# Kernel tuning notes

Measured on AMD Instinct MI355X. Metric: run time of the kernel, lower is better.

The kernel has to match this reference:

```python
import jax, jax.numpy as jnp
import numpy as np

BS, T, D, R = 8, 256, 2048, 4
N, K, G, GS, H = 8192, 64, 512, 16, 64
MOD_IN, MOD_OUT = K + 5, K + 2


def setup_inputs() -> dict:
    key = jax.random.key(0)
    ks = jax.random.split(key, 8)
    cc_signals = jax.random.normal(ks[0], (BS, T, D), dtype=jnp.float32)
    mod_w1 = jax.random.normal(ks[1], (G, MOD_IN, H), dtype=jnp.float32) * (2.0 / (MOD_IN + H)) ** 0.5
    mod_b1 = jnp.zeros((G, H), dtype=jnp.float32)
    mod_w2 = jax.random.normal(ks[2], (G, H, MOD_OUT), dtype=jnp.float32) * 0.01
    mod_b2 = jax.random.normal(ks[3], (G, MOD_OUT), dtype=jnp.float32) * 0.01
    conn_indices = jax.random.randint(ks[4], (N, K), 0, N, dtype=jnp.int32)
    conn_indices = jnp.sort(conn_indices, axis=-1)
    pos = jnp.arange(N, dtype=jnp.float32)
    neuron_id = jnp.stack([jnp.sin(pos * (2 * np.pi / N)), jnp.cos(pos * (2 * np.pi / N))], axis=-1)
    V0 = jax.random.normal(ks[5], (BS, N), dtype=jnp.float32) * 0.1
    activation0 = jax.nn.sigmoid(V0)
    hebbian0 = jnp.zeros((BS, N, K), dtype=jnp.float32)
    decay0 = jnp.full((BS, N), 0.9, dtype=jnp.float32)
    threshold0 = jnp.zeros((BS, N), dtype=jnp.float32)
    return {"cc_signals": cc_signals, "mod_w1": mod_w1, "mod_b1": mod_b1,
            "mod_w2": mod_w2, "mod_b2": mod_b2, "conn_indices": conn_indices,
            "neuron_id": neuron_id, "V0": V0, "activation0": activation0,
            "hebbian0": hebbian0, "decay0": decay0, "threshold0": threshold0}


def _modulator(activation, hebbian, decay, threshold, neuron_id, w1, b1, w2, b2):
    # [BS, N, K+5]
    nid = jnp.broadcast_to(neuron_id[None], (BS, N, 2))
    mod_in = jnp.concatenate([activation[..., None], hebbian, decay[..., None],
                              threshold[..., None], nid], axis=-1)
    x = mod_in.reshape(BS, G, GS, MOD_IN)
    hdn = jnp.tanh(jnp.einsum('bgsi,gih->bgsh', x, w1) + b1[None, :, None, :])
    out = jnp.einsum('bgsh,gho->bgso', hdn, w2) + b2[None, :, None, :]
    out = out.reshape(BS, N, MOD_OUT)
    return out[..., :K], jax.nn.sigmoid(out[..., K]), out[..., K + 1]


def reference(cc_signals, mod_w1, mod_b1, mod_w2, mod_b2, conn_indices, neuron_id,
              V0, activation0, hebbian0, decay0, threshold0):
    w_conn, decay, threshold = _modulator(activation0, hebbian0, decay0, threshold0,
                                          neuron_id, mod_w1, mod_b1, mod_w2, mod_b2)
    inject_all = jnp.repeat(cc_signals, R, axis=-1)  # [BS, T, N]

    def step(carry, inj_t):
        V, act, heb = carry
        nbr = act[:, conn_indices]                       # [BS, N, K] gather
        recv = jnp.sum(nbr * w_conn, axis=-1) + inj_t    # [BS, N]
        V = decay * V + (1.0 - decay) * recv
        act = jax.nn.sigmoid(V - threshold)
        heb = heb + act[..., None] * nbr
        return (V, act, heb), act

    heb_init = jnp.zeros((BS, N, K), dtype=V0.dtype)
    (_, _, _), acts = jax.lax.scan(step, (V0, activation0, heb_init),
                                   jnp.swapaxes(inject_all, 0, 1))
    act_all = jnp.swapaxes(acts, 0, 1)                   # [BS, T, N]
    mem_out = act_all.reshape(BS, T, D, R).mean(axis=-1)  # readout
    return mem_out
```

## Files before the change

### kernel.cpp

```cpp
#include <hip/hip_runtime.h>
#include <cstdint>
#include <cstddef>

#define BS 8
#define TT 256
#define DD 2048
#define NN 8192
#define KK 64
#define GG 512
#define GSZ 16
#define HH 64
#define MIN_ 69
#define MOUT_ 66
#define NSL 32
#define SLN 256
#define NW (NN/2)

typedef float    f32x4 __attribute__((ext_vector_type(4)));
typedef uint32_t u32x4 __attribute__((ext_vector_type(4)));

__global__ __launch_bounds__(256) void prep_kernel(
    const int* __restrict__ conn, int* __restrict__ ad_stored,
    unsigned char* __restrict__ inv2)
{
  const int gtid = blockIdx.x * 256 + threadIdx.x;
  const int n    = gtid >> 6;
  const int lane = gtid & 63;
  int idx  = conn[(size_t)n * KK + lane];
  int bank = (idx >> 1) & 31;
  unsigned key = ((unsigned)bank << 6) | (unsigned)lane;
  int rank = 0;
  #pragma unroll
  for (int i = 0; i < 64; ++i) {
    unsigned ki = (unsigned)__shfl((int)key, i);
    rank += (ki < key) ? 1 : 0;
  }
  const int ln = n & 63;
  const int r  = ((ln & 31) * 2 + (ln >> 5)) & 63;
  int j = (rank - r) & 63;
  ad_stored[(size_t)n * KK + j] = ((idx >> 1) << 2) | (idx & 1);
  inv2[(size_t)n * KK + lane]   = (unsigned char)j;
}

__global__ __launch_bounds__(256) void modulator_kernel(
    const float* __restrict__ w1, const float* __restrict__ b1,
    const float* __restrict__ w2, const float* __restrict__ b2,
    const float* __restrict__ act0, const float* __restrict__ heb0,
    const float* __restrict__ dec0, const float* __restrict__ thr0,
    const float* __restrict__ nid, const unsigned char* __restrict__ inv2,
    float* __restrict__ wconn, float* __restrict__ decayB, float* __restrict__ thrB)
{
  const int g = blockIdx.x, tid = threadIdx.x;
  __shared__ float w1s[MIN_ * HH];
  __shared__ float w2s[HH * MOUT_];
  __shared__ float b2s[MOUT_];
  __shared__ float xs[GSZ][MIN_];
  __shared__ float hd[GSZ * HH];

  for (int j = tid; j < MIN_ * HH; j += 256) w1s[j] = w1[(size_t)g * MIN_ * HH + j];
  for (int j = tid; j < HH * MOUT_; j += 256) w2s[j] = w2[(size_t)g * HH * MOUT_ + j];
  if (tid < MOUT_) b2s[tid] = b2[g * MOUT_ + tid];
  const float b1v = b1[g * HH + (tid & 63)];
  const int nbase = g * GSZ;

  for (int b = 0; b < BS; ++b) {
    __syncthreads();
    for (int j = tid; j < GSZ * KK; j += 256) {
      int s = j >> 6, k = j & 63;
      xs[s][1 + k] = heb0[((size_t)(b * NN + nbase + s)) * KK + k];
    }
    if (tid < GSZ) {
      int n = nbase + tid;
      xs[tid][0]  = act0[b * NN + n];
      xs[tid][65] = dec0[b * NN + n];
      xs[tid][66] = thr0[b * NN + n];
      xs[tid][67] = nid[2 * n];
      xs[tid][68] = nid[2 * n + 1];
    }
    __syncthreads();

    #pragma unroll
    for (int rep = 0; rep < 4; ++rep) {
      int s = rep * 4 + (tid >> 6), h = tid & 63;
      float acc = b1v;
      for (int i = 0; i < MIN_; ++i) acc = fmaf(xs[s][i], w1s[i * HH + h], acc);
      hd[s * HH + h] = tanhf(acc);
    }
    __syncthreads();

    for (int j = tid; j < GSZ * MOUT_; j += 256) {
      int s = j / MOUT_, o = j - s * MOUT_;
      float acc = b2s[o];
      for (int h = 0; h < HH; ++h) acc = fmaf(hd[s * HH + h], w2s[h * MOUT_ + o], acc);
      int nn = nbase + s;
      int gidx = b * NN + nn;
      if (o < KK) {
        int jp = inv2[(size_t)nn * KK + o];
        wconn[(size_t)gidx * KK + jp] = acc;
      }
      else if (o == KK) decayB[gidx] = 1.f / (1.f + expf(-acc));
      else              thrB[gidx]   = acc;
    }
  }
}

__global__ __launch_bounds__(256, 1) void scan_kernel(
    const float* __restrict__ cc, const int* __restrict__ ad_stored,
    const float* __restrict__ V0, const float* __restrict__ act0,
    const float* __restrict__ wconn, const float* __restrict__ decayB,
    const float* __restrict__ thrB,
    float* __restrict__ out, uint32_t* actbuf)
{
  const int tid = threadIdx.x;
  const int b   = blockIdx.x & 7;
  const int sl  = blockIdx.x >> 3;
  const int n    = sl * SLN + tid;
  const int gidx = b * NN + n;

  __shared__ uint32_t alds[NW];

  f32x4 w4[16];
  int   ad[KK];
  uint32_t mlo = 0, mhi = 0;
  {
    const f32x4* wr = reinterpret_cast<const f32x4*>(wconn + (size_t)gidx * KK);
    #pragma unroll
    for (int j = 0; j < 16; ++j) {
      f32x4 v = wr[j];
      w4[j] = v * (1.f / 4095.f);
    }
    const int4* ir = reinterpret_cast<const int4*>(ad_stored + (size_t)n * KK);
    #pragma unroll
    for (int j = 0; j < KK / 4; ++j) {
      int4 v = ir[j];
      ad[4*j+0] = v.x; ad[4*j+1] = v.y;
      ad[4*j+2] = v.z; ad[4*j+3] = v.w;
    }
    #pragma unroll
    for (int k = 0; k < 32; ++k) { mlo |= (uint32_t)(ad[k] & 1) << k;      ad[k] &= ~1; }
    #pragma unroll
    for (int k = 32; k < 64; ++k) { mhi |= (uint32_t)(ad[k] & 1) << (k-32); ad[k] &= ~1; }
  }
  float V     = V0[gidx];
  float dec   = decayB[gidx];
  float onemd = 1.f - dec;
  float thr   = thrB[gidx];

  for (int w = tid; w < NW; w += 256) {
    float a0 = act0[(size_t)b * NN + 2 * w];
    float a1 = act0[(size_t)b * NN + 2 * w + 1];
    uint32_t q0 = (uint32_t)__builtin_rintf(a0 * 4095.f);
    uint32_t q1 = (uint32_t)__builtin_rintf(a1 * 4095.f);
    alds[w] = (q1 << 12) | q0;
  }
  __syncthreads();

  float inj = cc[((size_t)b * TT) * DD + (n >> 2)];
  const char* abase = reinterpret_cast<const char*>(alds);

  for (int t = 0; t < TT; ++t) {
    float s0 = 0.f, s1 = 0.f, s2 = 0.f, s3 = 0.f;
    #pragma unroll
    for (int j = 0; j < 16; ++j) {
      uint32_t d0 = *reinterpret_cast<const uint32_t*>(abase + ad[4*j+0]);
      uint32_t d1 = *reinterpret_cast<const uint32_t*>(abase + ad[4*j+1]);
      uint32_t d2 = *reinterpret_cast<const uint32_t*>(abase + ad[4*j+2]);
      uint32_t d3 = *reinterpret_cast<const uint32_t*>(abase + ad[4*j+3]);
      uint32_t sh0, sh1, sh2, sh3;
      if (4*j+3 < 32) {
        sh0 = ((mlo >> (4*j+0)) & 1) * 12; sh1 = ((mlo >> (4*j+1)) & 1) * 12;
        sh2 = ((mlo >> (4*j+2)) & 1) * 12; sh3 = ((mlo >> (4*j+3)) & 1) * 12;
      } else {
        sh0 = ((mhi >> (4*j+0-32)) & 1) * 12; sh1 = ((mhi >> (4*j+1-32)) & 1) * 12;
        sh2 = ((mhi >> (4*j+2-32)) & 1) * 12; sh3 = ((mhi >> (4*j+3-32)) & 1) * 12;
      }
      s0 = fmaf((float)((d0 >> sh0) & 0xFFFu), w4[j].x, s0);
      s1 = fmaf((float)((d1 >> sh1) & 0xFFFu), w4[j].y, s1);
      s2 = fmaf((float)((d2 >> sh2) & 0xFFFu), w4[j].z, s2);
      s3 = fmaf((float)((d3 >> sh3) & 0xFFFu), w4[j].w, s3);
    }
    float recv = (s0 + s1) + (s2 + s3) + inj;
    V = dec * V + onemd * recv;
    float x = V - thr;
    float a = 1.f / (1.f + expf(-x));

    const int pw = t & 1;

    if (t != TT - 1) {
      uint32_t aq = (uint32_t)__builtin_rintf(a * 4095.f);
      uint32_t oq = (uint32_t)__shfl_xor((int)aq, 1);
      if ((tid & 1) == 0) {
        uint32_t word = ((uint32_t)(t + 1) << 24) | (oq << 12) | aq;
        uint32_t* dst = actbuf + (size_t)pw * (BS * NW) + (gidx >> 1);
        asm volatile("global_store_dword %0, %1, off sc0 sc1"
                     :: "v"(dst), "v"(word) : "memory");
      }
    }

    float p = a + __shfl_xor(a, 1);
    p = p + __shfl_xor(p, 2);
    if ((tid & 3) == 0)
      out[((size_t)b * TT + t) * DD + sl * 64 + (tid >> 2)] = 0.25f * p;

    if (t == TT - 1) break;

    inj = cc[((size_t)b * TT + t + 1) * DD + (n >> 2)];

    const uint32_t* src = actbuf + (size_t)pw * (BS * NW) + (size_t)b * NW;
    const uint32_t tag = (uint32_t)(t + 1);
    u32x4 vals[4];
    for (;;) {
      #pragma unroll
      for (int j = 0; j < 4; ++j) {
        const uint32_t* p4 = src + (tid << 2) + (j << 10);
        asm volatile("global_load_dwordx4 %0, %1, off sc0 sc1"
                     : "=v"(vals[j]) : "v"(p4));
      }
      asm volatile("s_waitcnt vmcnt(0)" ::: "memory");
      uint32_t bad = 0;
      #pragma unroll
      for (int j = 0; j < 4; ++j) {
        bad |= (vals[j].x >> 24) ^ tag;
        bad |= (vals[j].y >> 24) ^ tag;
        bad |= (vals[j].z >> 24) ^ tag;
        bad |= (vals[j].w >> 24) ^ tag;
      }
      if (bad == 0) break;
    }
    {
      u32x4* dst = reinterpret_cast<u32x4*>(alds);
      #pragma unroll
      for (int j = 0; j < 4; ++j) dst[tid + j * 256] = vals[j];
    }
    __syncthreads();
  }
}

extern "C" void kernel_launch(void* const* d_in, const int* in_sizes, int n_in,
                              void* d_out, int out_size, void* d_ws, size_t ws_size,
                              hipStream_t stream)
{
  const float* cc   = (const float*)d_in[0];
  const float* w1   = (const float*)d_in[1];
  const float* b1   = (const float*)d_in[2];
  const float* w2   = (const float*)d_in[3];
  const float* b2   = (const float*)d_in[4];
  const int*   conn = (const int*)d_in[5];
  const float* nid  = (const float*)d_in[6];
  const float* V0   = (const float*)d_in[7];
  const float* act0 = (const float*)d_in[8];
  const float* heb0 = (const float*)d_in[9];
  const float* dec0 = (const float*)d_in[10];
  const float* thr0 = (const float*)d_in[11];
  float* out = (float*)d_out;

  char* ws = (char*)d_ws;
  float*         wconn  = (float*)ws;
  float*         decayB = (float*)(ws + (size_t)BS * NN * KK * 4);
  float*         thrB   = decayB + BS * NN;
  uint32_t*      actbuf = (uint32_t*)(thrB + BS * NN);
  int*           ad_st  = (int*)(actbuf + 2 * BS * NW);
  unsigned char* inv2   = (unsigned char*)(ad_st + (size_t)NN * KK);

  hipMemsetAsync(actbuf, 0, 2 * BS * NW * sizeof(uint32_t), stream);

  prep_kernel<<<dim3(NN * KK / 256), 256, 0, stream>>>(conn, ad_st, inv2);
  modulator_kernel<<<dim3(GG), 256, 0, stream>>>(w1, b1, w2, b2, act0, heb0, dec0,
                                                 thr0, nid, inv2, wconn, decayB, thrB);
  scan_kernel<<<dim3(BS * NSL), 256, 0, stream>>>(cc, ad_st, V0, act0, wconn,
                                                  decayB, thrB, out, actbuf);
}
```

Measured before the change: 775.0 us.

## Add repair pass that swaps gather slots to reduce LDS bank conflicts

```diff
diff --git a/kernel.cpp b/kernel.cpp
--- a/kernel.cpp
+++ b/kernel.cpp
@@ -20,15 +20,14 @@
 typedef uint32_t u32x4 __attribute__((ext_vector_type(4)));
 
 __global__ __launch_bounds__(256) void prep_kernel(
-    const int* __restrict__ conn, int* __restrict__ ad_stored,
-    unsigned char* __restrict__ inv2)
+    const int* __restrict__ conn, int* __restrict__ ad_stored)
 {
   const int gtid = blockIdx.x * 256 + threadIdx.x;
   const int n    = gtid >> 6;
-  const int lane = gtid & 63;
-  int idx  = conn[(size_t)n * KK + lane];
+  const int k    = gtid & 63;
+  int idx  = conn[(size_t)n * KK + k];
   int bank = (idx >> 1) & 31;
-  unsigned key = ((unsigned)bank << 6) | (unsigned)lane;
+  unsigned key = ((unsigned)bank << 6) | (unsigned)k;
   int rank = 0;
   #pragma unroll
   for (int i = 0; i < 64; ++i) {
@@ -38,8 +37,50 @@
   const int ln = n & 63;
   const int r  = ((ln & 31) * 2 + (ln >> 5)) & 63;
   int j = (rank - r) & 63;
-  ad_stored[(size_t)n * KK + j] = ((idx >> 1) << 2) | (idx & 1);
-  inv2[(size_t)n * KK + lane]   = (unsigned char)j;
+  ad_stored[(size_t)n * KK + j] = (k << 16) | ((idx >> 1) << 2) | (idx & 1);
+}
+
+__global__ __launch_bounds__(64) void repair_kernel(
+    int* __restrict__ ad_stored, unsigned char* __restrict__ inv2)
+{
+  const int l = threadIdx.x;
+  const int n = blockIdx.x * 64 + l;
+  __shared__ int E[64][64];
+  __shared__ int H[64][32];
+
+  for (int j = 0; j < 64; ++j) E[j][l] = ad_stored[(size_t)n * KK + j];
+  for (int i = l; i < 64 * 32; i += 64) (&H[0][0])[i] = 0;
+  __syncthreads();
+  for (int j = 0; j < 64; ++j)
+    atomicAdd(&H[j][(E[j][l] >> 2) & 31], 1);
+  __syncthreads();
+
+  for (int pass = 0; pass < 3; ++pass) {
+    for (int j = 0; j < 64; ++j) {
+      int e  = E[j][l];
+      int b  = (e >> 2) & 31;
+      if (H[j][b] > 2) {
+        for (int d = 1; d < 64; ++d) {
+          int j2 = (j + d) & 63;
+          int e2 = E[j2][l];
+          int b2 = (e2 >> 2) & 31;
+          if (b2 != b && H[j2][b] <= 1 && H[j][b2] <= 1) {
+            atomicSub(&H[j][b], 1);  atomicAdd(&H[j2][b], 1);
+            atomicSub(&H[j2][b2], 1); atomicAdd(&H[j][b2], 1);
+            E[j][l] = e2; E[j2][l] = e;
+            break;
+          }
+        }
+      }
+    }
+    __syncthreads();
+  }
+
+  for (int j = 0; j < 64; ++j) {
+    int e = E[j][l];
+    ad_stored[(size_t)n * KK + j] = e & 0xFFFF;
+    inv2[(size_t)n * KK + (e >> 16)] = (unsigned char)j;
+  }
 }
 
 __global__ __launch_bounds__(256) void modulator_kernel(
@@ -264,7 +305,8 @@
 
   hipMemsetAsync(actbuf, 0, 2 * BS * NW * sizeof(uint32_t), stream);
 
-  prep_kernel<<<dim3(NN * KK / 256), 256, 0, stream>>>(conn, ad_st, inv2);
+  prep_kernel<<<dim3(NN * KK / 256), 256, 0, stream>>>(conn, ad_st);
+  repair_kernel<<<dim3(NN / 64), 64, 0, stream>>>(ad_st, inv2);
   modulator_kernel<<<dim3(GG), 256, 0, stream>>>(w1, b1, w2, b2, act0, heb0, dec0,
                                                  thr0, nid, inv2, wconn, decayB, thrB);
   scan_kernel<<<dim3(BS * NSL), 256, 0, stream>>>(cc, ad_st, V0, act0, wconn,
```

New measurement: 2.680 ms. 3.46x slower.
